# Kernel optimization log

Measured on AMD Instinct MI355X. Metric: run time of the kernel, lower is better.

The kernel has to match this reference:

```python
import jax, jax.numpy as jnp
import numpy as np

N = 50000
E = 800000
C_IN, C_HID, C_OUT = 512, 128, 2
HEADS2 = 3
NEG_SLOPE = 0.2


def gat_conv(x, src, dst, W, att_src, att_dst, bias, heads, ch, concat):
    """PyG GATConv (eval mode) on pre-augmented (self-loop included) edge lists.
    x: [N, F_in], W: [F_in, heads*ch], att_*: [heads, ch], bias: [heads*ch] or [ch].
    """
    n = x.shape[0]
    h = (x @ W).reshape(n, heads, ch)                 # [N, H, C]
    a_src = (h * att_src).sum(-1)                     # [N, H]
    a_dst = (h * att_dst).sum(-1)                     # [N, H]
    e = jax.nn.leaky_relu(a_src[src] + a_dst[dst], NEG_SLOPE)  # [E', H]
    # segment softmax over edges sharing a destination node
    m = jax.ops.segment_max(e, dst, num_segments=n)
    m = jnp.where(jnp.isfinite(m), m, 0.0)
    ex = jnp.exp(e - m[dst])
    denom = jax.ops.segment_sum(ex, dst, num_segments=n)
    alpha = ex / (denom[dst] + 1e-16)                 # [E', H]
    out = jax.ops.segment_sum(h[src] * alpha[:, :, None], dst, num_segments=n)  # [N, H, C]
    out = out.reshape(n, heads * ch) if concat else out.mean(axis=1)
    return out + bias


def setup_inputs() -> dict:
    key = jax.random.key(0)
    ks = jax.random.split(key, 12)
    x = jax.random.normal(ks[0], (N, C_IN), dtype=jnp.float32)
    edge_index = jax.random.randint(ks[1], (2, E), 0, N, dtype=jnp.int64)
    s1 = 1.0 / np.sqrt(C_IN)
    s2 = 1.0 / np.sqrt(C_HID)
    return {
        "x": x,
        "edge_index": edge_index,
        "W1": jax.random.normal(ks[2], (C_IN, C_HID), dtype=jnp.float32) * s1,
        "att_src1": jax.random.normal(ks[3], (1, C_HID), dtype=jnp.float32) * s2,
        "att_dst1": jax.random.normal(ks[4], (1, C_HID), dtype=jnp.float32) * s2,
        "bias1": jnp.zeros((C_HID,), dtype=jnp.float32),
        "W2": jax.random.normal(ks[5], (C_HID, HEADS2 * C_OUT), dtype=jnp.float32) * s2,
        "att_src2": jax.random.normal(ks[6], (HEADS2, C_OUT), dtype=jnp.float32) * 0.5,
        "att_dst2": jax.random.normal(ks[7], (HEADS2, C_OUT), dtype=jnp.float32) * 0.5,
        "bias2": jnp.zeros((C_OUT,), dtype=jnp.float32),
    }


def reference(x, edge_index, W1, att_src1, att_dst1, bias1, W2, att_src2, att_dst2, bias2):
    n = x.shape[0]
    loop = jnp.arange(n, dtype=edge_index.dtype)
    src = jnp.concatenate([edge_index[0], loop])      # PyG add_self_loops=True
    dst = jnp.concatenate([edge_index[1], loop])
    h = gat_conv(x, src, dst, W1, att_src1, att_dst1, bias1, 1, C_HID, True)
    h = jax.nn.relu(h)                                # Dropout is identity in eval
    out = gat_conv(h, src, dst, W2, att_src2, att_dst2, bias2, HEADS2, C_OUT, False)
    return out
```

## Files before the change

### kernel.cpp

```cpp
#include <hip/hip_runtime.h>

#define N_NODES 50000
#define N_EDGES 800000
#define E_TOT   850000
#define C_IN    512
#define C_HID   128
#define NEG     0.2f

typedef _Float16 f16x8 __attribute__((ext_vector_type(8)));
typedef __attribute__((ext_vector_type(4))) float f32x4;

__device__ __forceinline__ float leaky(float x) { return x > 0.f ? x : NEG * x; }

union U32H2 { unsigned u; _Float16 h[2]; float f; };
union BFrag { uint4 u; f16x8 h; };

__device__ __forceinline__ unsigned short f2h(float f) {
  U32H2 c; c.h[0] = (_Float16)f; return (unsigned short)(c.u & 0xffff);
}

__device__ __forceinline__ unsigned pk2h(float a, float b) {
  union { __fp16 v __attribute__((ext_vector_type(2))); unsigned u; } c;
  c.v = __builtin_amdgcn_cvt_pkrtz(a, b);
  return c.u;
}

__device__ __forceinline__ float row_reduce_add(float v) {
  union { float f; int i; } a, b;
  a.f = v;
  b.i = __builtin_amdgcn_update_dpp(0, a.i, 0xB1, 0xF, 0xF, true);  a.f += b.f;
  b.i = __builtin_amdgcn_update_dpp(0, a.i, 0x4E, 0xF, 0xF, true);  a.f += b.f;
  b.i = __builtin_amdgcn_update_dpp(0, a.i, 0x124, 0xF, 0xF, true); a.f += b.f;
  b.i = __builtin_amdgcn_update_dpp(0, a.i, 0x128, 0xF, 0xF, true); a.f += b.f;
  return a.f;
}

__global__ __launch_bounds__(256) void setup_kernel(
    const float* __restrict__ W1, const float* __restrict__ as1,
    const float* __restrict__ ad1, const int* __restrict__ ei,
    unsigned short* __restrict__ Wswz, float* __restrict__ v1s, float* __restrict__ v1d,
    int* __restrict__ deg, int* __restrict__ rnk) {
  const int b = blockIdx.x;
  if (b < 32) {
    int t = b * 256 + threadIdx.x;
    int c = t >> 6, kc = t & 63;
    if (c >= C_HID) return;
    int kblk = kc >> 2, q = kc & 3;
    int ct = c >> 4, l15 = c & 15;
    int lane = q * 16 + l15;
    unsigned short hb[8], lb[8];
#pragma unroll
    for (int i = 0; i < 8; i++) {
      float w = W1[(size_t)(kc * 8 + i) * C_HID + c];
      _Float16 hi = (_Float16)w;
      _Float16 lo = (_Float16)(w - (float)hi);
      U32H2 ch; ch.h[0] = hi;
      U32H2 cl; cl.h[0] = lo;
      hb[i] = (unsigned short)(ch.u & 0xffff);
      lb[i] = (unsigned short)(cl.u & 0xffff);
    }
    size_t chunk0 = ((size_t)(kblk * 8 + ct) * 2) * 512;
    *(uint4*)&Wswz[chunk0 + (size_t)lane * 8]       = *(uint4*)hb;
    *(uint4*)&Wswz[chunk0 + 512 + (size_t)lane * 8] = *(uint4*)lb;
  } else if (b < 160) {
    const int wv = threadIdx.x >> 6, lane = threadIdx.x & 63;
    const int k = (b - 32) * 4 + wv;
    if (k >= C_IN) return;
    float2 w = *(const float2*)(W1 + (size_t)k * C_HID + 2 * lane);
    float2 a = *(const float2*)(as1 + 2 * lane);
    float2 d = *(const float2*)(ad1 + 2 * lane);
    float s = w.x * a.x + w.y * a.y;
    float t = w.x * d.x + w.y * d.y;
#pragma unroll
    for (int m = 32; m >= 1; m >>= 1) {
      s += __shfl_xor(s, m, 64);
      t += __shfl_xor(t, m, 64);
    }
    if (lane == 0) { v1s[k] = s; v1d[k] = t; }
  } else {
    int e = (b - 160) * 256 + threadIdx.x;
    if (e < N_EDGES) rnk[e] = atomicAdd(&deg[ei[N_EDGES + e]], 1);
  }
}

__global__ __launch_bounds__(256) void lin1_kernel(const float* __restrict__ x,
    const unsigned short* __restrict__ Wswz,
    const float* __restrict__ v1s, const float* __restrict__ v1d,
    unsigned short* __restrict__ h1u, float* __restrict__ a_src, float* __restrict__ a_dst,
    const int* __restrict__ deg, int* __restrict__ rowptr) {
  __shared__ __attribute__((aligned(16))) unsigned short As[2][2][64][40];
  __shared__ int wsum[4];

  if (blockIdx.x == 0) {
    const int tid = threadIdx.x, lane = tid & 63, wv = tid >> 6;
    int carry = 0;
    for (int base = 0; base < N_NODES; base += 8192) {
      int i0 = base + tid * 32;
      int v[32];
      if (i0 + 32 <= N_NODES) {
#pragma unroll
        for (int k = 0; k < 8; k++) {
          int4 t4 = *(const int4*)(deg + i0 + 4 * k);
          v[4 * k]     = t4.x + 1; v[4 * k + 1] = t4.y + 1;
          v[4 * k + 2] = t4.z + 1; v[4 * k + 3] = t4.w + 1;
        }
      } else {
#pragma unroll
        for (int k = 0; k < 32; k++) v[k] = (i0 + k < N_NODES) ? deg[i0 + k] + 1 : 0;
      }
      int tsum = 0;
#pragma unroll
      for (int k = 0; k < 32; k++) tsum += v[k];
      int sc = tsum;
#pragma unroll
      for (int off = 1; off < 64; off <<= 1) {
        int t = __shfl_up(sc, off, 64);
        if (lane >= off) sc += t;
      }
      if (lane == 63) wsum[wv] = sc;
      __syncthreads();
      if (tid < 4) {
        int s = wsum[tid];
#pragma unroll
        for (int off = 1; off < 4; off <<= 1) {
          int t = __shfl_up(s, off, 64);
          if (tid >= off) s += t;
        }
        wsum[tid] = s;
      }
      __syncthreads();
      int run = carry + (wv ? wsum[wv - 1] : 0) + sc - tsum;
      if (i0 + 32 <= N_NODES) {
#pragma unroll
        for (int k = 0; k < 8; k++) {
          int4 w4;
          w4.x = run; run += v[4 * k];
          w4.y = run; run += v[4 * k + 1];
          w4.z = run; run += v[4 * k + 2];
          w4.w = run; run += v[4 * k + 3];
          *(int4*)(rowptr + i0 + 4 * k) = w4;
        }
      } else {
#pragma unroll
        for (int k = 0; k < 32; k++) {
          if (i0 + k < N_NODES) rowptr[i0 + k] = run;
          run += v[k];
        }
      }
      carry += wsum[3];
      __syncthreads();
    }
    if (tid == 0) rowptr[N_NODES] = carry;
    return;
  }

  const int tid  = threadIdx.x;
  const int lane = tid & 63, wv = tid >> 6;
  const int m0   = (blockIdx.x - 1) * 64;

  const int arow = tid >> 2, kseg = (tid & 3) * 8;
  int grow = m0 + arow;
  if (grow >= N_NODES) grow = N_NODES - 1;
  const float* xrow = x + (size_t)grow * C_IN + kseg;

  f32x4 acc[4][2];
#pragma unroll
  for (int rt = 0; rt < 4; rt++) { acc[rt][0] = (f32x4)0.f; acc[rt][1] = (f32x4)0.f; }
  float ps = 0.f, pd = 0.f;

  const int q = lane >> 4, l15 = lane & 15;

  float4 xa0 = *(const float4*)(xrow);
  float4 xb0 = *(const float4*)(xrow + 4);
  float4 xa1 = *(const float4*)(xrow + 32);
  float4 xb1 = *(const float4*)(xrow + 36);

#pragma unroll
  for (int kb = 0; kb < 8; kb++) {
    const int k0 = kb * 64;
    const int buf = kb & 1;
    {
      float4 vsa = *(const float4*)(v1s + k0 + kseg);
      float4 vsb = *(const float4*)(v1s + k0 + kseg + 4);
      float4 vda = *(const float4*)(v1d + k0 + kseg);
      float4 vdb = *(const float4*)(v1d + k0 + kseg + 4);
      ps += xa0.x * vsa.x + xa0.y * vsa.y + xa0.z * vsa.z + xa0.w * vsa.w
          + xb0.x * vsb.x + xb0.y * vsb.y + xb0.z * vsb.z + xb0.w * vsb.w;
      pd += xa0.x * vda.x + xa0.y * vda.y + xa0.z * vda.z + xa0.w * vda.w
          + xb0.x * vdb.x + xb0.y * vdb.y + xb0.z * vdb.z + xb0.w * vdb.w;
      float4 vsc = *(const float4*)(v1s + k0 + 32 + kseg);
      float4 vsd = *(const float4*)(v1s + k0 + 32 + kseg + 4);
      float4 vdc = *(const float4*)(v1d + k0 + 32 + kseg);
      float4 vdd = *(const float4*)(v1d + k0 + 32 + kseg + 4);
      ps += xa1.x * vsc.x + xa1.y * vsc.y + xa1.z * vsc.z + xa1.w * vsc.w
          + xb1.x * vsd.x + xb1.y * vsd.y + xb1.z * vsd.z + xb1.w * vsd.w;
      pd += xa1.x * vdc.x + xa1.y * vdc.y + xa1.z * vdc.z + xa1.w * vdc.w
          + xb1.x * vdd.x + xb1.y * vdd.y + xb1.z * vdd.z + xb1.w * vdd.w;
    }
    *(uint4*)&As[buf][0][arow][kseg] = make_uint4(pk2h(xa0.x, xa0.y), pk2h(xa0.z, xa0.w),
                                                  pk2h(xb0.x, xb0.y), pk2h(xb0.z, xb0.w));
    *(uint4*)&As[buf][1][arow][kseg] = make_uint4(pk2h(xa1.x, xa1.y), pk2h(xa1.z, xa1.w),
                                                  pk2h(xb1.x, xb1.y), pk2h(xb1.z, xb1.w));
    __syncthreads();
    if (kb < 7) {
      xa0 = *(const float4*)(xrow + k0 + 64);
      xb0 = *(const float4*)(xrow + k0 + 68);
      xa1 = *(const float4*)(xrow + k0 + 96);
      xb1 = *(const float4*)(xrow + k0 + 100);
    }

    const unsigned short* bp0 = Wswz + ((size_t)((kb * 2) * 8 + wv * 2) * 2) * 512 + (size_t)lane * 8;
    const unsigned short* bp1 = Wswz + ((size_t)((kb * 2 + 1) * 8 + wv * 2) * 2) * 512 + (size_t)lane * 8;
    BFrag s0b00, s0b01, s0b10, s0b11, s1b00, s1b01, s1b10, s1b11;
    s0b00.u = *(const uint4*)(bp0);
    s0b01.u = *(const uint4*)(bp0 + 512);
    s0b10.u = *(const uint4*)(bp0 + 1024);
    s0b11.u = *(const uint4*)(bp0 + 1536);
    s1b00.u = *(const uint4*)(bp1);
    s1b01.u = *(const uint4*)(bp1 + 512);
    s1b10.u = *(const uint4*)(bp1 + 1024);
    s1b11.u = *(const uint4*)(bp1 + 1536);

#pragma unroll
    for (int rt = 0; rt < 4; rt++) {
      f16x8 af0 = *(const f16x8*)&As[buf][0][rt * 16 + l15][q * 8];
      acc[rt][0] = __builtin_amdgcn_mfma_f32_16x16x32_f16(af0, s0b00.h, acc[rt][0], 0, 0, 0);
      acc[rt][0] = __builtin_amdgcn_mfma_f32_16x16x32_f16(af0, s0b01.h, acc[rt][0], 0, 0, 0);
      acc[rt][1] = __builtin_amdgcn_mfma_f32_16x16x32_f16(af0, s0b10.h, acc[rt][1], 0, 0, 0);
      acc[rt][1] = __builtin_amdgcn_mfma_f32_16x16x32_f16(af0, s0b11.h, acc[rt][1], 0, 0, 0);
      f16x8 af1 = *(const f16x8*)&As[buf][1][rt * 16 + l15][q * 8];
      acc[rt][0] = __builtin_amdgcn_mfma_f32_16x16x32_f16(af1, s1b00.h, acc[rt][0], 0, 0, 0);
      acc[rt][0] = __builtin_amdgcn_mfma_f32_16x16x32_f16(af1, s1b01.h, acc[rt][0], 0, 0, 0);
      acc[rt][1] = __builtin_amdgcn_mfma_f32_16x16x32_f16(af1, s1b10.h, acc[rt][1], 0, 0, 0);
      acc[rt][1] = __builtin_amdgcn_mfma_f32_16x16x32_f16(af1, s1b11.h, acc[rt][1], 0, 0, 0);
    }
  }

  ps += __shfl_xor(ps, 1, 64); ps += __shfl_xor(ps, 2, 64);
  pd += __shfl_xor(pd, 1, 64); pd += __shfl_xor(pd, 2, 64);
  if ((tid & 3) == 0) {
    int row = m0 + arow;
    if (row < N_NODES) { a_src[row] = ps; a_dst[row] = pd; }
  }

#pragma unroll
  for (int rt = 0; rt < 4; rt++) {
    int rbase = m0 + rt * 16 + q * 4;
#pragma unroll
    for (int ct = 0; ct < 2; ct++) {
      int col = wv * 32 + ct * 16 + l15;
#pragma unroll
      for (int ri = 0; ri < 4; ri++) {
        int row = rbase + ri;
        if (row < N_NODES)
          h1u[(size_t)row * C_HID + col] = f2h(acc[rt][ct][ri]);
      }
    }
  }
}

__global__ void bucket_kernel(const int* __restrict__ ei, const int* __restrict__ rnk,
                              const int* __restrict__ rowptr,
                              const float* __restrict__ a_src, const float* __restrict__ a_dst,
                              int2* __restrict__ esw) {
  int e = blockIdx.x * blockDim.x + threadIdx.x;
  if (e >= E_TOT) return;
  int src, slot;
  if (e < N_EDGES) {
    src = ei[e];
    int dst = ei[N_EDGES + e];
    slot = rowptr[dst] + rnk[e];
    U32H2 c; c.f = __expf(leaky(a_src[src] + a_dst[dst]));
    esw[slot] = make_int2(src, (int)c.u);
  } else {
    int n = e - N_EDGES;
    slot = rowptr[n + 1] - 1;
    U32H2 c; c.f = __expf(leaky(a_src[n] + a_dst[n]));
    esw[slot] = make_int2(n, (int)c.u);
  }
}

__global__ __launch_bounds__(256) void agg1_kernel(const unsigned short* __restrict__ h1u,
    const int2* __restrict__ esw, const int* __restrict__ rowptr,
    const float* __restrict__ bias1, const float* __restrict__ W2,
    const float* __restrict__ as2w, const float* __restrict__ ad2w,
    float* __restrict__ hs2) {
  const int wv = threadIdx.x >> 6, lane = threadIdx.x & 63;
  const int r = lane & 15;
  const int n = blockIdx.x * 16 + wv * 4 + (lane >> 4);
  const int start = rowptr[n], end = rowptr[n + 1];

  const unsigned short* hbase = h1u + r * 8;

  float acc[8] = {0, 0, 0, 0, 0, 0, 0, 0};
  float wsum = 0.f;

  int base = start;
  int cnt = min(end - base, 8);
  int2 rec[8];
#pragma unroll
  for (int j = 0; j < 8; j++) rec[j] = esw[j < cnt ? base + j : base];

  while (true) {
    const int nbase = base + 8;
    const bool more = nbase < end;
    int ncnt = 0;
    int2 nrec[8];
    if (more) {
      ncnt = min(end - nbase, 8);
#pragma unroll
      for (int j = 0; j < 8; j++) nrec[j] = esw[j < ncnt ? nbase + j : nbase];
    }
    uint4 g[8];
#pragma unroll
    for (int j = 0; j < 8; j++)
      g[j] = *(const uint4*)(hbase + (size_t)rec[j].x * C_HID);
#pragma unroll
    for (int j = 0; j < 8; j++) {
      U32H2 cw; cw.u = (unsigned)rec[j].y;
      const float W = (j < cnt) ? cw.f : 0.f;
      wsum += W;
      U32H2 c0, c1, c2, c3;
      c0.u = g[j].x; c1.u = g[j].y; c2.u = g[j].z; c3.u = g[j].w;
      acc[0] = fmaf(W, (float)c0.h[0], acc[0]); acc[1] = fmaf(W, (float)c0.h[1], acc[1]);
      acc[2] = fmaf(W, (float)c1.h[0], acc[2]); acc[3] = fmaf(W, (float)c1.h[1], acc[3]);
      acc[4] = fmaf(W, (float)c2.h[0], acc[4]); acc[5] = fmaf(W, (float)c2.h[1], acc[5]);
      acc[6] = fmaf(W, (float)c3.h[0], acc[6]); acc[7] = fmaf(W, (float)c3.h[1], acc[7]);
    }
    if (!more) break;
    base = nbase; cnt = ncnt;
#pragma unroll
    for (int j = 0; j < 8; j++) rec[j] = nrec[j];
  }

  const float inv = 1.f / wsum;

  float4 ba = *(const float4*)(bias1 + r * 8);
  float4 bb = *(const float4*)(bias1 + r * 8 + 4);
  float u[8] = {fmaxf(acc[0] * inv + ba.x, 0.f), fmaxf(acc[1] * inv + ba.y, 0.f),
                fmaxf(acc[2] * inv + ba.z, 0.f), fmaxf(acc[3] * inv + ba.w, 0.f),
                fmaxf(acc[4] * inv + bb.x, 0.f), fmaxf(acc[5] * inv + bb.y, 0.f),
                fmaxf(acc[6] * inv + bb.z, 0.f), fmaxf(acc[7] * inv + bb.w, 0.f)};
  float p[6] = {0, 0, 0, 0, 0, 0};
#pragma unroll
  for (int j = 0; j < 8; j++) {
    const float* w2r = W2 + (size_t)(r * 8 + j) * 6;
#pragma unroll
    for (int o = 0; o < 6; o++) p[o] = fmaf(u[j], w2r[o], p[o]);
  }
#pragma unroll
  for (int o = 0; o < 6; o++) p[o] = row_reduce_add(p[o]);

  if (r == 0) {
    float as0 = p[0] * as2w[0] + p[1] * as2w[1];
    float as1 = p[2] * as2w[2] + p[3] * as2w[3];
    float as2_ = p[4] * as2w[4] + p[5] * as2w[5];
    float ad0 = p[0] * ad2w[0] + p[1] * ad2w[1];
    float ad1 = p[2] * ad2w[2] + p[3] * ad2w[3];
    float ad2_ = p[4] * ad2w[4] + p[5] * ad2w[5];
    float* dst = hs2 + (size_t)n * 12;
    *(float4*)(dst)     = make_float4(p[0], p[1], p[2], p[3]);
    *(float4*)(dst + 4) = make_float4(p[4], p[5], as0, as1);
    *(float4*)(dst + 8) = make_float4(as2_, ad0, ad1, ad2_);
  }
}

__global__ __launch_bounds__(256) void agg2_kernel(const float* __restrict__ hs2,
    const int* __restrict__ rowptr, const int2* __restrict__ esw,
    const float* __restrict__ bias2, float* __restrict__ out) {
  const int wv = threadIdx.x >> 6, lane = threadIdx.x & 63;
  const int q = lane >> 4, r = lane & 15;
  const int n = blockIdx.x * 16 + wv * 4 + q;
  if (n >= N_NODES) return;
  const int start = rowptr[n], end = rowptr[n + 1];
  float4 own = *(const float4*)(hs2 + (size_t)n * 12 + 8);
  const float ad0 = own.y, ad1 = own.z, ad2 = own.w;

  float d0 = 0.f, d1 = 0.f, d2 = 0.f;
  float a0 = 0.f, a1 = 0.f, a2 = 0.f, a3 = 0.f, a4 = 0.f, a5 = 0.f;
  for (int j = start + r; j < end; j += 16) {
    int s = esw[j].x;
    const float* rec = hs2 + (size_t)s * 12;
    float4 A = *(const float4*)(rec);
    float4 B = *(const float4*)(rec + 4);
    float  C = rec[8];
    float e0 = __expf(leaky(B.z + ad0));
    float e1 = __expf(leaky(B.w + ad1));
    float e2 = __expf(leaky(C + ad2));
    d0 += e0; d1 += e1; d2 += e2;
    a0 += e0 * A.x; a1 += e0 * A.y;
    a2 += e1 * A.z; a3 += e1 * A.w;
    a4 += e2 * B.x; a5 += e2 * B.y;
  }
  d0 = row_reduce_add(d0); d1 = row_reduce_add(d1); d2 = row_reduce_add(d2);
  a0 = row_reduce_add(a0); a1 = row_reduce_add(a1); a2 = row_reduce_add(a2);
  a3 = row_reduce_add(a3); a4 = row_reduce_add(a4); a5 = row_reduce_add(a5);
  if (r == 0) {
    float o0 = (a0 / d0 + a2 / d1 + a4 / d2) * (1.f / 3.f) + bias2[0];
    float o1 = (a1 / d0 + a3 / d1 + a5 / d2) * (1.f / 3.f) + bias2[1];
    *(float2*)(out + (size_t)n * 2) = make_float2(o0, o1);
  }
}

extern "C" void kernel_launch(void* const* d_in, const int* in_sizes, int n_in,
                              void* d_out, int out_size, void* d_ws, size_t ws_size,
                              hipStream_t stream) {
  const float* x        = (const float*)d_in[0];
  const int*   ei       = (const int*)d_in[1];
  const float* W1       = (const float*)d_in[2];
  const float* att_src1 = (const float*)d_in[3];
  const float* att_dst1 = (const float*)d_in[4];
  const float* bias1    = (const float*)d_in[5];
  const float* W2       = (const float*)d_in[6];
  const float* att_src2 = (const float*)d_in[7];
  const float* att_dst2 = (const float*)d_in[8];
  const float* bias2    = (const float*)d_in[9];
  float* out = (float*)d_out;

  char* w = (char*)d_ws;
  auto alloc = [&](size_t bytes) {
    char* p = w;
    w += (bytes + 255) & ~(size_t)255;
    return p;
  };
  unsigned short* h1u    = (unsigned short*)alloc((size_t)N_NODES * C_HID * 2);
  unsigned short* Wswz   = (unsigned short*)alloc((size_t)C_IN * C_HID * 2 * 2);
  float*          v1s    = (float*)alloc((size_t)C_IN * 4);
  float*          v1d    = (float*)alloc((size_t)C_IN * 4);
  float*          a_src1 = (float*)alloc((size_t)N_NODES * 4);
  float*          a_dst1 = (float*)alloc((size_t)N_NODES * 4);
  int*            deg    = (int*)alloc((size_t)N_NODES * 4);
  int*            rowptr = (int*)alloc((size_t)(N_NODES + 4) * 4);
  int*            rnk    = (int*)alloc((size_t)N_EDGES * 4);
  int2*           esw    = (int2*)alloc((size_t)E_TOT * 8);
  float*          hs2    = (float*)alloc((size_t)N_NODES * 12 * 4);

  (void)hipMemsetAsync(deg, 0, (size_t)N_NODES * 4, stream);

  setup_kernel<<<160 + (N_EDGES + 255) / 256, 256, 0, stream>>>(
      W1, att_src1, att_dst1, ei, Wswz, v1s, v1d, deg, rnk);
  lin1_kernel<<<(N_NODES + 63) / 64 + 1, 256, 0, stream>>>(x, Wswz, v1s, v1d,
                                                           h1u, a_src1, a_dst1,
                                                           deg, rowptr);
  bucket_kernel<<<(E_TOT + 255) / 256, 256, 0, stream>>>(ei, rnk, rowptr,
                                                         a_src1, a_dst1, esw);
  agg1_kernel<<<N_NODES / 16, 256, 0, stream>>>(h1u, esw, rowptr, bias1, W2,
                                                att_src2, att_dst2, hs2);
  agg2_kernel<<<(N_NODES + 15) / 16, 256, 0, stream>>>(hs2, rowptr, esw, bias2, out);
}
```

Before: 291.9 us.

## Overlap degree counting with the GEMM inside lin1 via a completion counter

Moves the per-edge degree and rank atomics out of the setup kernel and into dedicated blocks of the lin1 kernel, so they run alongside the GEMM blocks. The prefix-scan block, scheduled last, spin-waits on a device-scope counter until all degree blocks finish. One memset now clears both the degree array and the counter, and launch bounds add an occupancy hint of 3 blocks. The scan block relies on forward progress of earlier-indexed blocks, and the scan now uses scalar atomic loads in place of vectorized loads.

Measured after the change: 310.3 us. +6.3%, slower.

```diff
diff --git a/kernel.cpp b/kernel.cpp
--- a/kernel.cpp
+++ b/kernel.cpp
@@ -6,6 +6,9 @@
 #define C_IN    512
 #define C_HID   128
 #define NEG     0.2f
+
+#define DR_BLKS   256
+#define GEMM_BLKS 782
 
 typedef _Float16 f16x8 __attribute__((ext_vector_type(8)));
 typedef __attribute__((ext_vector_type(4))) float f32x4;
@@ -37,9 +40,8 @@
 
 __global__ __launch_bounds__(256) void setup_kernel(
     const float* __restrict__ W1, const float* __restrict__ as1,
-    const float* __restrict__ ad1, const int* __restrict__ ei,
-    unsigned short* __restrict__ Wswz, float* __restrict__ v1s, float* __restrict__ v1d,
-    int* __restrict__ deg, int* __restrict__ rnk) {
+    const float* __restrict__ ad1,
+    unsigned short* __restrict__ Wswz, float* __restrict__ v1s, float* __restrict__ v1d) {
   const int b = blockIdx.x;
   if (b < 32) {
     int t = b * 256 + threadIdx.x;
@@ -62,7 +64,7 @@
     size_t chunk0 = ((size_t)(kblk * 8 + ct) * 2) * 512;
     *(uint4*)&Wswz[chunk0 + (size_t)lane * 8]       = *(uint4*)hb;
     *(uint4*)&Wswz[chunk0 + 512 + (size_t)lane * 8] = *(uint4*)lb;
-  } else if (b < 160) {
+  } else {
     const int wv = threadIdx.x >> 6, lane = threadIdx.x & 63;
     const int k = (b - 32) * 4 + wv;
     if (k >= C_IN) return;
@@ -77,36 +79,46 @@
       t += __shfl_xor(t, m, 64);
     }
     if (lane == 0) { v1s[k] = s; v1d[k] = t; }
-  } else {
-    int e = (b - 160) * 256 + threadIdx.x;
-    if (e < N_EDGES) rnk[e] = atomicAdd(&deg[ei[N_EDGES + e]], 1);
-  }
-}
-
-__global__ __launch_bounds__(256) void lin1_kernel(const float* __restrict__ x,
+  }
+}
+
+__global__ __launch_bounds__(256, 3) void lin1_kernel(const float* __restrict__ x,
     const unsigned short* __restrict__ Wswz,
     const float* __restrict__ v1s, const float* __restrict__ v1d,
     unsigned short* __restrict__ h1u, float* __restrict__ a_src, float* __restrict__ a_dst,
-    const int* __restrict__ deg, int* __restrict__ rowptr) {
+    int* __restrict__ deg, int* __restrict__ rowptr,
+    const int* __restrict__ ei, int* __restrict__ rnk, int* __restrict__ dctr) {
   __shared__ __attribute__((aligned(16))) unsigned short As[2][2][64][40];
   __shared__ int wsum[4];
 
-  if (blockIdx.x == 0) {
+  const int b = blockIdx.x;
+
+  if (b < DR_BLKS) {
+    const int tid = threadIdx.x;
+    for (int e = b * 256 + tid; e < N_EDGES; e += DR_BLKS * 256)
+      rnk[e] = atomicAdd(&deg[ei[N_EDGES + e]], 1);
+    __syncthreads();
+    if (tid == 0) { __threadfence(); atomicAdd(dctr, 1); }
+    return;
+  }
+
+  if (b == DR_BLKS + GEMM_BLKS) {
     const int tid = threadIdx.x, lane = tid & 63, wv = tid >> 6;
+    if (tid == 0) {
+      while (__hip_atomic_load(dctr, __ATOMIC_ACQUIRE, __HIP_MEMORY_SCOPE_AGENT) < DR_BLKS)
+        __builtin_amdgcn_s_sleep(32);
+    }
+    __syncthreads();
     int carry = 0;
     for (int base = 0; base < N_NODES; base += 8192) {
       int i0 = base + tid * 32;
       int v[32];
-      if (i0 + 32 <= N_NODES) {
-#pragma unroll
-        for (int k = 0; k < 8; k++) {
-          int4 t4 = *(const int4*)(deg + i0 + 4 * k);
-          v[4 * k]     = t4.x + 1; v[4 * k + 1] = t4.y + 1;
-          v[4 * k + 2] = t4.z + 1; v[4 * k + 3] = t4.w + 1;
-        }
-      } else {
-#pragma unroll
-        for (int k = 0; k < 32; k++) v[k] = (i0 + k < N_NODES) ? deg[i0 + k] + 1 : 0;
+#pragma unroll
+      for (int k = 0; k < 32; k++) {
+        int idx = i0 + k;
+        v[k] = (idx < N_NODES)
+            ? __hip_atomic_load(&deg[idx], __ATOMIC_RELAXED, __HIP_MEMORY_SCOPE_AGENT) + 1
+            : 0;
       }
       int tsum = 0;
 #pragma unroll
@@ -156,7 +168,7 @@
 
   const int tid  = threadIdx.x;
   const int lane = tid & 63, wv = tid >> 6;
-  const int m0   = (blockIdx.x - 1) * 64;
+  const int m0   = (b - DR_BLKS) * 64;
 
   const int arow = tid >> 2, kseg = (tid & 3) * 8;
   int grow = m0 + arow;
@@ -430,18 +442,17 @@
   float*          a_src1 = (float*)alloc((size_t)N_NODES * 4);
   float*          a_dst1 = (float*)alloc((size_t)N_NODES * 4);
   int*            deg    = (int*)alloc((size_t)N_NODES * 4);
+  int*            dctr   = (int*)alloc(256);
   int*            rowptr = (int*)alloc((size_t)(N_NODES + 4) * 4);
   int*            rnk    = (int*)alloc((size_t)N_EDGES * 4);
   int2*           esw    = (int2*)alloc((size_t)E_TOT * 8);
   float*          hs2    = (float*)alloc((size_t)N_NODES * 12 * 4);
 
-  (void)hipMemsetAsync(deg, 0, (size_t)N_NODES * 4, stream);
-
-  setup_kernel<<<160 + (N_EDGES + 255) / 256, 256, 0, stream>>>(
-      W1, att_src1, att_dst1, ei, Wswz, v1s, v1d, deg, rnk);
-  lin1_kernel<<<(N_NODES + 63) / 64 + 1, 256, 0, stream>>>(x, Wswz, v1s, v1d,
-                                                           h1u, a_src1, a_dst1,
-                                                           deg, rowptr);
+  (void)hipMemsetAsync(deg, 0, (((size_t)N_NODES * 4 + 255) & ~(size_t)255) + 256, stream);
+
+  setup_kernel<<<160, 256, 0, stream>>>(W1, att_src1, att_dst1, Wswz, v1s, v1d);
+  lin1_kernel<<<DR_BLKS + GEMM_BLKS + 1, 256, 0, stream>>>(
+      x, Wswz, v1s, v1d, h1u, a_src1, a_dst1, deg, rowptr, ei, rnk, dctr);
   bucket_kernel<<<(E_TOT + 255) / 256, 256, 0, stream>>>(ei, rnk, rowptr,
                                                          a_src1, a_dst1, esw);
   agg1_kernel<<<N_NODES / 16, 256, 0, stream>>>(h1u, esw, rowptr, bias1, W2,
```
